# Kernel optimization log

Measured on AMD Instinct MI355X. Metric: run time of the kernel, lower is better.

The kernel has to match this reference:

```python
import jax, jax.numpy as jnp
import numpy as np

B, S, D = 4, 2048, 1024
H = 16
DH = D // H
MLP_DIM = 4096
EPS = 1e-6


def setup_inputs() -> dict:
    key = jax.random.key(0)
    ks = jax.random.split(key, 16)
    sd = lambda fi, fo: (1.0 / np.sqrt(fi))
    return {
        "x": jax.random.normal(ks[0], (B, S, D), jnp.float32),
        "Wq": jax.random.normal(ks[1], (D, D), jnp.float32) * sd(D, D),
        "bq": jnp.zeros((D,), jnp.float32),
        "Wk": jax.random.normal(ks[2], (D, D), jnp.float32) * sd(D, D),
        "bk": jnp.zeros((D,), jnp.float32),
        "Wv": jax.random.normal(ks[3], (D, D), jnp.float32) * sd(D, D),
        "bv": jnp.zeros((D,), jnp.float32),
        "Wo": jax.random.normal(ks[4], (D, D), jnp.float32) * sd(D, D),
        "bo": jnp.zeros((D,), jnp.float32),
        "ln1_g": jnp.ones((D,), jnp.float32),
        "ln1_b": jnp.zeros((D,), jnp.float32),
        "ln2_g": jnp.ones((D,), jnp.float32),
        "ln2_b": jnp.zeros((D,), jnp.float32),
        "W1": jax.random.normal(ks[5], (D, MLP_DIM), jnp.float32) * sd(D, MLP_DIM),
        "b1": jax.random.normal(ks[6], (MLP_DIM,), jnp.float32) * 1e-6,
        "W2": jax.random.normal(ks[7], (MLP_DIM, D), jnp.float32) * sd(MLP_DIM, D),
        "b2": jax.random.normal(ks[8], (D,), jnp.float32) * 1e-6,
    }


def _layernorm(x, g, b):
    mu = jnp.mean(x, axis=-1, keepdims=True)
    var = jnp.mean(jnp.square(x - mu), axis=-1, keepdims=True)
    return (x - mu) * jax.lax.rsqrt(var + EPS) * g + b


def reference(x, Wq, bq, Wk, bk, Wv, bv, Wo, bo,
              ln1_g, ln1_b, ln2_g, ln2_b, W1, b1, W2, b2):
    h = x
    xn = _layernorm(x, ln1_g, ln1_b)
    # Q/K/V: [B,S,D] -> [B,H,S,DH]
    def split_heads(t):
        return t.reshape(B, S, H, DH).transpose(0, 2, 1, 3)
    Q = split_heads(xn @ Wq + bq)
    K = split_heads(xn @ Wk + bk)
    V = split_heads(xn @ Wv + bv)
    scores = jnp.einsum("bhqd,bhkd->bhqk", Q, K) / np.sqrt(DH).astype(np.float32)
    a = jax.nn.softmax(scores, axis=-1)
    r = jnp.einsum("bhqk,bhkd->bhqd", a, V)          # [B,H,S,DH]
    r = r.transpose(0, 2, 1, 3).reshape(B, S, D)      # merge heads
    r = r @ Wo + bo
    x = r + h
    h = x
    xn = _layernorm(x, ln2_g, ln2_b)
    m = jax.nn.gelu(xn @ W1 + b1, approximate=False)
    m = m @ W2 + b2
    return m + h
```

## Files before the change

kernel.cpp:

```cpp
#include <hip/hip_runtime.h>
#include <math.h>

#define B_ 4
#define S_ 2048
#define D_ 1024
#define H_ 16
#define MLP_ 4096
#define MROWS 8192

typedef __attribute__((ext_vector_type(4))) float f32x4;
typedef __attribute__((ext_vector_type(16))) float f32x16;
typedef __attribute__((ext_vector_type(8))) __bf16 bf16x8;
typedef __attribute__((ext_vector_type(4))) __bf16 bf16x4;
typedef __attribute__((ext_vector_type(8))) unsigned short us8;
typedef unsigned short u16;
typedef unsigned int u32;

__device__ __forceinline__ void gload16(const void* g, void* l) {
    __builtin_amdgcn_global_load_lds((const __attribute__((address_space(1))) u32*)g,
                                     (__attribute__((address_space(3))) u32*)l, 16, 0, 0);
}

__device__ __forceinline__ float gelu_f(float v) {
    return 0.5f * v * (1.0f + erff(v * 0.70710678118654752f));
}

__global__ __launch_bounds__(256) void ln_bf16_k(const float* __restrict__ x,
                                                 const float* __restrict__ g,
                                                 const float* __restrict__ b,
                                                 u16* __restrict__ y) {
    int row = blockIdx.x;
    int tid = threadIdx.x;
    const float* xr = x + (size_t)row * D_;
    f32x4 v = *(const f32x4*)(xr + tid * 4);
    float s = v.x + v.y + v.z + v.w;
    float ss = v.x * v.x + v.y * v.y + v.z * v.z + v.w * v.w;
    for (int off = 32; off > 0; off >>= 1) {
        s += __shfl_down(s, off, 64);
        ss += __shfl_down(ss, off, 64);
    }
    __shared__ float rs[4], rss[4];
    int lane = tid & 63, wid = tid >> 6;
    if (lane == 0) { rs[wid] = s; rss[wid] = ss; }
    __syncthreads();
    s = rs[0] + rs[1] + rs[2] + rs[3];
    ss = rss[0] + rss[1] + rss[2] + rss[3];
    float mu = s * (1.0f / D_);
    float var = ss * (1.0f / D_) - mu * mu;
    float inv = rsqrtf(var + 1e-6f);
    f32x4 gg = *(const f32x4*)(g + tid * 4);
    f32x4 bb = *(const f32x4*)(b + tid * 4);
    bf16x4 o = {(__bf16)((v.x - mu) * inv * gg.x + bb.x),
                (__bf16)((v.y - mu) * inv * gg.y + bb.y),
                (__bf16)((v.z - mu) * inv * gg.z + bb.z),
                (__bf16)((v.w - mu) * inv * gg.w + bb.w)};
    *(bf16x4*)(y + (size_t)row * D_ + tid * 4) = o;
}

__global__ void pack3_k(const float* __restrict__ a, const float* __restrict__ b,
                        const float* __restrict__ c, float* __restrict__ o) {
    const float* s = blockIdx.x == 0 ? a : (blockIdx.x == 1 ? b : c);
    o[blockIdx.x * 1024 + threadIdx.x] = s[threadIdx.x];
}

__global__ __launch_bounds__(256) void wtrans_k(const float* __restrict__ W,
                                                u16* __restrict__ Wt, int K, int N) {
    __shared__ float T[32][33];
    int tid = threadIdx.x;
    int k0 = blockIdx.y * 32, n0 = blockIdx.x * 32;
    int r = tid >> 3, c4 = (tid & 7) * 4;
    f32x4 v = *(const f32x4*)&W[(size_t)(k0 + r) * N + n0 + c4];
    T[r][c4 + 0] = v.x; T[r][c4 + 1] = v.y; T[r][c4 + 2] = v.z; T[r][c4 + 3] = v.w;
    __syncthreads();
    int n = tid >> 3, kk = (tid & 7) * 4;
    bf16x4 o = {(__bf16)T[kk + 0][n], (__bf16)T[kk + 1][n],
                (__bf16)T[kk + 2][n], (__bf16)T[kk + 3][n]};
    *(bf16x4*)&Wt[(size_t)(n0 + n) * K + k0 + kk] = o;
}

__global__ __launch_bounds__(256) void vtrans_k(const u16* __restrict__ QKV,
                                                u16* __restrict__ Vt) {
    __shared__ u16 T[64][80];
    int tid = threadIdx.x;
    int s0 = blockIdx.x * 64;
    int bh = blockIdx.y, b = bh >> 4, h = bh & 15;
    int r = tid >> 2, c0 = (tid & 3) * 16;
    const u16* src = QKV + (size_t)(b * S_ + s0 + r) * 3072 + 2048 + h * 64 + c0;
    us8 v0 = *(const us8*)src;
    us8 v1 = *(const us8*)(src + 8);
    *(us8*)&T[r][c0] = v0;
    *(us8*)&T[r][c0 + 8] = v1;
    __syncthreads();
    int dh = tid >> 2, s8 = (tid & 3) * 16;
    us8 o0, o1;
#pragma unroll
    for (int i = 0; i < 8; ++i) { o0[i] = T[s8 + i][dh]; o1[i] = T[s8 + 8 + i][dh]; }
    u16* dst = Vt + (size_t)(bh * 64 + dh) * S_ + s0 + s8;
    *(us8*)dst = o0;
    *(us8*)(dst + 8) = o1;
}

template <int EPI>
__global__ __launch_bounds__(256) void gemm_bf16(const u16* __restrict__ A,
                                                 const u16* __restrict__ Wt,
                                                 const float* __restrict__ bias,
                                                 const float* __restrict__ res,
                                                 void* __restrict__ Cout,
                                                 int M, int N, int K) {
    __shared__ u16 As[3][128 * 32];
    __shared__ u16 Bs[3][128 * 32];
    const int tid = threadIdx.x;
    const int lane = tid & 63;
    const int w = tid >> 6;
    const int nwg = gridDim.x * gridDim.y;
    int hw = blockIdx.x + gridDim.x * blockIdx.y;
    int lg = (hw & 7) * (nwg >> 3) + (hw >> 3);
    const int row0 = (lg / gridDim.x) * 128;
    const int col0 = (lg % gridDim.x) * 128;
    const int l15 = lane & 15, l16 = lane >> 4;
    const int wr = w >> 1, wc = w & 1;

    f32x4 acc[4][4];
#pragma unroll
    for (int i = 0; i < 4; ++i)
#pragma unroll
        for (int j = 0; j < 4; ++j) acc[i][j] = (f32x4){0.f, 0.f, 0.f, 0.f};

    const int srow = w * 32 + (lane >> 2);
    const size_t sboff = (size_t)(lane & 3) * 16;
    const char* Ag = (const char*)A + ((size_t)(row0 + srow) * K) * 2 + sboff;
    const char* Bg = (const char*)Wt + ((size_t)(col0 + srow) * K) * 2 + sboff;
    const size_t rstep = (size_t)16 * K * 2;
    const int woff = w * 2048;
    const int T = K >> 5;

#define STAGE(t, bi) do {                                      \
        size_t kb = (size_t)(t) << 6;                          \
        char* asw = (char*)As + (bi) * 8192 + woff;            \
        char* bsw = (char*)Bs + (bi) * 8192 + woff;            \
        gload16(Ag + kb, asw);                                 \
        gload16(Ag + kb + rstep, asw + 1024);                  \
        gload16(Bg + kb, bsw);                                 \
        gload16(Bg + kb + rstep, bsw + 1024);                  \
    } while (0)

    STAGE(0, 0);
    STAGE(1, 1);
    asm volatile("s_waitcnt vmcnt(4)" ::: "memory");
    __builtin_amdgcn_s_barrier();
    __builtin_amdgcn_sched_barrier(0);

    int bi = 0;
    for (int t = 0; t < T; ++t) {
        if (t + 2 < T) {
            int nb = bi + 2; if (nb >= 3) nb -= 3;
            STAGE(t + 2, nb);
        }
        const char* Ab = (const char*)As + bi * 8192;
        const char* Bb = (const char*)Bs + bi * 8192;
        bf16x8 af[4], bfr[4];
#pragma unroll
        for (int f = 0; f < 4; ++f) {
            af[f] = *(const bf16x8*)(Ab + (size_t)(wr * 64 + f * 16 + l15) * 64 + (l16 << 4));
            bfr[f] = *(const bf16x8*)(Bb + (size_t)(wc * 64 + f * 16 + l15) * 64 + (l16 << 4));
        }
        __builtin_amdgcn_s_setprio(1);
#pragma unroll
        for (int fi = 0; fi < 4; ++fi)
#pragma unroll
            for (int fj = 0; fj < 4; ++fj)
                acc[fi][fj] = __builtin_amdgcn_mfma_f32_16x16x32_bf16(af[fi], bfr[fj], acc[fi][fj], 0, 0, 0);
        __builtin_amdgcn_s_setprio(0);
        if (t + 2 < T) {
            asm volatile("s_waitcnt vmcnt(4)" ::: "memory");
        } else {
            asm volatile("s_waitcnt vmcnt(0)" ::: "memory");
        }
        __builtin_amdgcn_s_barrier();
        __builtin_amdgcn_sched_barrier(0);
        if (++bi >= 3) bi = 0;
    }
#undef STAGE

    const int rb = row0 + wr * 64 + (l16 << 2);
    const int cb = col0 + wc * 64 + l15;
#pragma unroll
    for (int fi = 0; fi < 4; ++fi)
#pragma unroll
        for (int fj = 0; fj < 4; ++fj) {
            int c = cb + fj * 16;
            float bv = bias[c];
#pragma unroll
            for (int rr = 0; rr < 4; ++rr) {
                int r = rb + fi * 16 + rr;
                float v = acc[fi][fj][rr] + bv;
                if (EPI == 1) v = gelu_f(v);
                if (EPI == 2) {
                    v += res[(size_t)r * N + c];
                    ((float*)Cout)[(size_t)r * N + c] = v;
                } else {
                    ((__bf16*)Cout)[(size_t)r * N + c] = (__bf16)v;
                }
            }
        }
}

__global__ __launch_bounds__(256) void attn_mfma(const u16* __restrict__ QKV,
                                                 const u16* __restrict__ Vt,
                                                 u16* __restrict__ O) {
    __shared__ u16 Ks[2][64 * 64];
    __shared__ u16 Vs[2][64 * 64];
    __shared__ u16 Ps[4][32 * 64];
    const int tid = threadIdx.x, lane = tid & 63, w = tid >> 6;
    int hw = blockIdx.x + gridDim.x * blockIdx.y;
    int lg = (hw & 7) * 128 + (hw >> 3);
    const int bh = lg >> 4, b = bh >> 4, h = bh & 15;
    const int q0 = (lg & 15) * 128;
    const int l31 = lane & 31, lh = lane >> 5;

    const u16* Qp = QKV + (size_t)(b * S_ + q0 + w * 32 + l31) * 3072 + h * 64 + lh * 8;
    bf16x8 qf[4];
    qf[0] = *(const bf16x8*)(Qp);
    qf[1] = *(const bf16x8*)(Qp + 16);
    qf[2] = *(const bf16x8*)(Qp + 32);
    qf[3] = *(const bf16x8*)(Qp + 48);

    f32x16 oacc[2];
#pragma unroll
    for (int i = 0; i < 16; ++i) { oacc[0][i] = 0.f; oacc[1][i] = 0.f; }
    float mold = -1e30f, lsum = 0.f;

    const int sr = lane >> 3;
    const size_t soff = (size_t)(((lane & 7) ^ sr) << 4);
    const char* Kg = (const char*)QKV + ((size_t)b * S_ * 3072 + 1024 + h * 64) * 2;
    const char* Vg = (const char*)Vt + (size_t)bh * 64 * S_ * 2;
    char* Pw = (char*)Ps[w];
    const int sw = (l31 & 7) << 4;
    const float C2 = 0.18033688011112f;
    const float THRRAW = 44.0f;

    const char* kp0 = Kg + (size_t)(w * 16 + sr) * 6144 + soff;
    const char* kp1 = kp0 + 8 * 6144;
    const char* vp0 = Vg + (size_t)(w * 16 + sr) * 4096 + soff;
    const char* vp1 = vp0 + 8 * 4096;
    const size_t KADV = 64 * 6144;
    const size_t VADV = 128;
    char* ksA = (char*)Ks[0] + w * 2048;
    char* ksB = (char*)Ks[1] + w * 2048;
    char* vsA = (char*)Vs[0] + w * 2048;
    char* vsB = (char*)Vs[1] + w * 2048;

    gload16(kp0, ksA); gload16(kp1, ksA + 1024);
    gload16(vp0, vsA); gload16(vp1, vsA + 1024);
    kp0 += KADV; kp1 += KADV; vp0 += VADV; vp1 += VADV;
    __syncthreads();

    for (int kt = 0; kt < S_ / 64; ++kt) {
        const int cur = kt & 1;
        if (kt < S_ / 64 - 1) {
            char* kd = cur ? ksA : ksB;
            char* vd = cur ? vsA : vsB;
            gload16(kp0, kd); gload16(kp1, kd + 1024);
            gload16(vp0, vd); gload16(vp1, vd + 1024);
            kp0 += KADV; kp1 += KADV; vp0 += VADV; vp1 += VADV;
        }

        const char* Kb_ = (const char*)Ks[cur];
        f32x16 sfr[2];
        __builtin_amdgcn_s_setprio(1);
#pragma unroll
        for (int kh = 0; kh < 2; ++kh) {
            int r = kh * 32 + l31;
            int rsw = (r & 7) << 4;
            const char* Kr = Kb_ + r * 128;
            f32x16 t;
#pragma unroll
            for (int i = 0; i < 16; ++i) t[i] = 0.f;
#pragma unroll
            for (int ds = 0; ds < 4; ++ds) {
                bf16x8 kf = *(const bf16x8*)(Kr + ((((ds * 2 + lh) << 4)) ^ rsw));
                t = __builtin_amdgcn_mfma_f32_32x32x16_bf16(kf, qf[ds], t, 0, 0, 0);
            }
            sfr[kh] = t;
        }
        __builtin_amdgcn_s_setprio(0);

        float mx = fmaxf(sfr[0][0], sfr[1][0]);
#pragma unroll
        for (int i = 1; i < 16; ++i) mx = fmaxf(mx, fmaxf(sfr[0][i], sfr[1][i]));
        mx = fmaxf(mx, __shfl_xor(mx, 32, 64));

        bool need = mx > mold + THRRAW;
        if (__any(need)) {
            float mnew = fmaxf(mold, mx);
            float al = exp2f((mold - mnew) * C2);
            lsum *= al;
            mold = mnew;
#pragma unroll
            for (int i = 0; i < 16; ++i) { oacc[0][i] *= al; oacc[1][i] *= al; }
        }

        float nm = -mold * C2;
        float pv0[16], pv1[16];
        float psum = 0.f;
#pragma unroll
        for (int i = 0; i < 16; ++i) {
            pv0[i] = exp2f(fmaf(sfr[0][i], C2, nm));
            pv1[i] = exp2f(fmaf(sfr[1][i], C2, nm));
            psum += pv0[i] + pv1[i];
        }
        psum += __shfl_xor(psum, 32, 64);
        lsum += psum;

        {
            char* Pr = Pw + l31 * 128;
#pragma unroll
            for (int t4 = 0; t4 < 4; ++t4) {
                int kb0 = (t4 * 8 + lh * 4) * 2;
                bf16x4 pa = {(__bf16)pv0[t4 * 4], (__bf16)pv0[t4 * 4 + 1],
                             (__bf16)pv0[t4 * 4 + 2], (__bf16)pv0[t4 * 4 + 3]};
                bf16x4 pb = {(__bf16)pv1[t4 * 4], (__bf16)pv1[t4 * 4 + 1],
                             (__bf16)pv1[t4 * 4 + 2], (__bf16)pv1[t4 * 4 + 3]};
                *(bf16x4*)(Pr + (kb0 ^ sw)) = pa;
                *(bf16x4*)(Pr + ((kb0 + 64) ^ sw)) = pb;
            }
        }

        {
            const char* Vb_ = (const char*)Vs[cur];
            const char* Pr = Pw + l31 * 128;
            bf16x8 pf[4];
#pragma unroll
            for (int ks = 0; ks < 4; ++ks)
                pf[ks] = *(const bf16x8*)(Pr + ((((ks * 2 + lh) << 4)) ^ sw));
            __builtin_amdgcn_s_setprio(1);
#pragma unroll
            for (int dh = 0; dh < 2; ++dh) {
                int r = dh * 32 + l31;
                int rsw = (r & 7) << 4;
                const char* Vr = Vb_ + r * 128;
#pragma unroll
                for (int ks = 0; ks < 4; ++ks) {
                    bf16x8 vf = *(const bf16x8*)(Vr + ((((ks * 2 + lh) << 4)) ^ rsw));
                    oacc[dh] = __builtin_amdgcn_mfma_f32_32x32x16_bf16(vf, pf[ks], oacc[dh], 0, 0, 0);
                }
            }
            __builtin_amdgcn_s_setprio(0);
        }
        __syncthreads();
    }

    float invl = 1.0f / lsum;
    char* Og = (char*)O + ((size_t)(b * S_ + q0 + w * 32 + l31) * 1024 + h * 64) * 2;
#pragma unroll
    for (int dh = 0; dh < 2; ++dh)
#pragma unroll
        for (int t4 = 0; t4 < 4; ++t4) {
            int db = dh * 32 + t4 * 8 + lh * 4;
            bf16x4 ov = {(__bf16)(oacc[dh][t4 * 4] * invl),
                         (__bf16)(oacc[dh][t4 * 4 + 1] * invl),
                         (__bf16)(oacc[dh][t4 * 4 + 2] * invl),
                         (__bf16)(oacc[dh][t4 * 4 + 3] * invl)};
            *(bf16x4*)(Og + db * 2) = ov;
        }
}

extern "C" void kernel_launch(void* const* d_in, const int* in_sizes, int n_in,
                              void* d_out, int out_size, void* d_ws, size_t ws_size,
                              hipStream_t stream) {
    const float* x     = (const float*)d_in[0];
    const float* Wq    = (const float*)d_in[1];
    const float* bq    = (const float*)d_in[2];
    const float* Wk    = (const float*)d_in[3];
    const float* bk    = (const float*)d_in[4];
    const float* Wv    = (const float*)d_in[5];
    const float* bv    = (const float*)d_in[6];
    const float* Wo    = (const float*)d_in[7];
    const float* bo    = (const float*)d_in[8];
    const float* ln1_g = (const float*)d_in[9];
    const float* ln1_b = (const float*)d_in[10];
    const float* ln2_g = (const float*)d_in[11];
    const float* ln2_b = (const float*)d_in[12];
    const float* W1    = (const float*)d_in[13];
    const float* b1    = (const float*)d_in[14];
    const float* W2    = (const float*)d_in[15];
    const float* b2    = (const float*)d_in[16];
    float* out = (float*)d_out;

    const size_t MB = 1ull << 20;
    char* ws = (char*)d_ws;
    u16* QKVb = (u16*)(ws + 0 * MB);
    u16* aout = (u16*)(ws + 48 * MB);
    u16* mid  = (u16*)(ws + 0 * MB);
    float* x2 = (float*)(ws + 64 * MB);
    float* bqkv = (float*)(ws + 64 * MB);
    u16* xn   = (u16*)(ws + 96 * MB);
    u16* Vt   = (u16*)(ws + 96 * MB);
    u16* xn2  = (u16*)(ws + 96 * MB);
    u16* Wqkvt = (u16*)(ws + 112 * MB);
    u16* Wot  = Wqkvt + (size_t)3072 * D_;
    u16* W1t  = (u16*)(ws + 112 * MB);
    u16* W2t  = (u16*)(ws + 120 * MB);

    wtrans_k<<<dim3(32, 32), 256, 0, stream>>>(Wq, Wqkvt, D_, D_);
    wtrans_k<<<dim3(32, 32), 256, 0, stream>>>(Wk, Wqkvt + (size_t)D_ * D_, D_, D_);
    wtrans_k<<<dim3(32, 32), 256, 0, stream>>>(Wv, Wqkvt + (size_t)2 * D_ * D_, D_, D_);
    wtrans_k<<<dim3(32, 32), 256, 0, stream>>>(Wo, Wot, D_, D_);
    wtrans_k<<<dim3(32, 128), 256, 0, stream>>>(W2, W2t, MLP_, D_);
    pack3_k<<<3, 1024, 0, stream>>>(bq, bk, bv, bqkv);

    ln_bf16_k<<<MROWS, 256, 0, stream>>>(x, ln1_g, ln1_b, xn);
    gemm_bf16<0><<<dim3(24, 64), 256, 0, stream>>>(xn, Wqkvt, bqkv, nullptr, QKVb, MROWS, 3072, D_);
    vtrans_k<<<dim3(32, 64), 256, 0, stream>>>(QKVb, Vt);
    attn_mfma<<<dim3(16, 64), 256, 0, stream>>>(QKVb, Vt, aout);
    gemm_bf16<2><<<dim3(8, 64), 256, 0, stream>>>(aout, Wot, bo, x, x2, MROWS, D_, D_);
    wtrans_k<<<dim3(128, 32), 256, 0, stream>>>(W1, W1t, D_, MLP_);
    ln_bf16_k<<<MROWS, 256, 0, stream>>>(x2, ln2_g, ln2_b, xn2);
    gemm_bf16<1><<<dim3(32, 64), 256, 0, stream>>>(xn2, W1t, b1, nullptr, mid, MROWS, MLP_, D_);
    gemm_bf16<2><<<dim3(8, 64), 256, 0, stream>>>(mid, W2t, b2, x2, (void*)out, MROWS, D_, MLP_);
}
```

Baseline: 504.0 us.

## Keep softmax P in registers by permuting V layout, drop LDS round-trip

```diff
diff --git a/kernel.cpp b/kernel.cpp
--- a/kernel.cpp
+++ b/kernel.cpp
@@ -78,6 +78,9 @@
     *(bf16x4*)&Wt[(size_t)(n0 + n) * K + k0 + kk] = o;
 }
 
+__device__ __forceinline__ int sigma_perm(int s) {
+    return (s & 48) | (s & 3) | (((s >> 2) & 1) << 3) | (((s >> 3) & 1) << 2);
+}
 __global__ __launch_bounds__(256) void vtrans_k(const u16* __restrict__ QKV,
                                                 u16* __restrict__ Vt) {
     __shared__ u16 T[64][80];
@@ -94,7 +97,10 @@
     int dh = tid >> 2, s8 = (tid & 3) * 16;
     us8 o0, o1;
 #pragma unroll
-    for (int i = 0; i < 8; ++i) { o0[i] = T[s8 + i][dh]; o1[i] = T[s8 + 8 + i][dh]; }
+    for (int i = 0; i < 8; ++i) {
+        o0[i] = T[sigma_perm(s8 + i)][dh];
+        o1[i] = T[sigma_perm(s8 + 8 + i)][dh];
+    }
     u16* dst = Vt + (size_t)(bh * 64 + dh) * S_ + s0 + s8;
     *(us8*)dst = o0;
     *(us8*)(dst + 8) = o1;
@@ -210,7 +216,6 @@
                                                  u16* __restrict__ O) {
     __shared__ u16 Ks[2][64 * 64];
     __shared__ u16 Vs[2][64 * 64];
-    __shared__ u16 Ps[4][32 * 64];
     const int tid = threadIdx.x, lane = tid & 63, w = tid >> 6;
     int hw = blockIdx.x + gridDim.x * blockIdx.y;
     int lg = (hw & 7) * 128 + (hw >> 3);
@@ -234,8 +239,6 @@
     const size_t soff = (size_t)(((lane & 7) ^ sr) << 4);
     const char* Kg = (const char*)QKV + ((size_t)b * S_ * 3072 + 1024 + h * 64) * 2;
     const char* Vg = (const char*)Vt + (size_t)bh * 64 * S_ * 2;
-    char* Pw = (char*)Ps[w];
-    const int sw = (l31 & 7) << 4;
     const float C2 = 0.18033688011112f;
     const float THRRAW = 44.0f;
 
@@ -293,7 +296,7 @@
         bool need = mx > mold + THRRAW;
         if (__any(need)) {
             float mnew = fmaxf(mold, mx);
-            float al = exp2f((mold - mnew) * C2);
+            float al = __builtin_amdgcn_exp2f((mold - mnew) * C2);
             lsum *= al;
             mold = mnew;
 #pragma unroll
@@ -305,34 +308,24 @@
         float psum = 0.f;
 #pragma unroll
         for (int i = 0; i < 16; ++i) {
-            pv0[i] = exp2f(fmaf(sfr[0][i], C2, nm));
-            pv1[i] = exp2f(fmaf(sfr[1][i], C2, nm));
+            pv0[i] = __builtin_amdgcn_exp2f(fmaf(sfr[0][i], C2, nm));
+            pv1[i] = __builtin_amdgcn_exp2f(fmaf(sfr[1][i], C2, nm));
             psum += pv0[i] + pv1[i];
         }
         psum += __shfl_xor(psum, 32, 64);
         lsum += psum;
 
-        {
-            char* Pr = Pw + l31 * 128;
-#pragma unroll
-            for (int t4 = 0; t4 < 4; ++t4) {
-                int kb0 = (t4 * 8 + lh * 4) * 2;
-                bf16x4 pa = {(__bf16)pv0[t4 * 4], (__bf16)pv0[t4 * 4 + 1],
-                             (__bf16)pv0[t4 * 4 + 2], (__bf16)pv0[t4 * 4 + 3]};
-                bf16x4 pb = {(__bf16)pv1[t4 * 4], (__bf16)pv1[t4 * 4 + 1],
-                             (__bf16)pv1[t4 * 4 + 2], (__bf16)pv1[t4 * 4 + 3]};
-                *(bf16x4*)(Pr + (kb0 ^ sw)) = pa;
-                *(bf16x4*)(Pr + ((kb0 + 64) ^ sw)) = pb;
-            }
+        bf16x8 pf[4];
+#pragma unroll
+        for (int j = 0; j < 8; ++j) {
+            pf[0][j] = (__bf16)pv0[j];
+            pf[1][j] = (__bf16)pv0[8 + j];
+            pf[2][j] = (__bf16)pv1[j];
+            pf[3][j] = (__bf16)pv1[8 + j];
         }
 
         {
             const char* Vb_ = (const char*)Vs[cur];
-            const char* Pr = Pw + l31 * 128;
-            bf16x8 pf[4];
-#pragma unroll
-            for (int ks = 0; ks < 4; ++ks)
-                pf[ks] = *(const bf16x8*)(Pr + ((((ks * 2 + lh) << 4)) ^ sw));
             __builtin_amdgcn_s_setprio(1);
 #pragma unroll
             for (int dh = 0; dh < 2; ++dh) {
```

After: 465.1 us. 1.08x faster.
